# Kernel optimization log

Measured on AMD Instinct MI355X. Metric: run time of the kernel, lower is better.

The kernel has to match this reference:

```python
import jax, jax.numpy as jnp
import numpy as np

B, CIN, K, H, W = 8, 256, 128, 112, 112


def setup_inputs() -> dict:
    key = jax.random.key(0)
    k1, k2, k3, k4 = jax.random.split(key, 4)
    return {
        "x": jax.random.normal(k1, (B, CIN, H, W), jnp.float32),
        "linComb": jax.random.uniform(k2, (K, CIN), dtype=jnp.float32),
        "geoParams": jax.random.uniform(k3, (K, 2, 3), dtype=jnp.float32),
        "boxParams": jax.random.uniform(k4, (K, 2, 3), dtype=jnp.float32),
    }


def _affine_sample(img, theta):
    """F.affine_grid + F.grid_sample (bilinear, zeros padding, align_corners=False).
    img: [B, K, H, W] (one feature channel per geometric channel k)
    theta: [K, 2, 3] affine params, shared across batch.
    """
    Bn, Kn, Hn, Wn = img.shape
    # normalized output coords (align_corners=False pixel centers)
    xs = (2.0 * jnp.arange(Wn, dtype=img.dtype) + 1.0) / Wn - 1.0
    ys = (2.0 * jnp.arange(Hn, dtype=img.dtype) + 1.0) / Hn - 1.0
    gxv, gyv = jnp.meshgrid(xs, ys)  # [H, W]
    coords = jnp.stack([gxv, gyv, jnp.ones_like(gxv)], axis=-1)  # [H, W, 3]
    grid = jnp.einsum('kij,hwj->khwi', theta, coords)  # [K, H, W, 2] (x, y)
    # unnormalize to input pixel space
    ix = ((grid[..., 0] + 1.0) * Wn - 1.0) * 0.5
    iy = ((grid[..., 1] + 1.0) * Hn - 1.0) * 0.5
    x0 = jnp.floor(ix)
    y0 = jnp.floor(iy)
    wx1 = ix - x0
    wx0 = 1.0 - wx1
    wy1 = iy - y0
    wy0 = 1.0 - wy1
    imgf = img.reshape(Bn, Kn, Hn * Wn)

    def gather(xc, yc, w):
        valid = (xc >= 0) & (xc <= Wn - 1) & (yc >= 0) & (yc <= Hn - 1)
        xi = jnp.clip(xc, 0, Wn - 1).astype(jnp.int32)
        yi = jnp.clip(yc, 0, Hn - 1).astype(jnp.int32)
        idx = (yi * Wn + xi).reshape(Kn, Hn * Wn)
        vals = jnp.take_along_axis(
            imgf, jnp.broadcast_to(idx[None], (Bn, Kn, Hn * Wn)), axis=2
        ).reshape(Bn, Kn, Hn, Wn)
        return vals * (w * valid.astype(img.dtype))[None]

    out = (gather(x0, y0, wx0 * wy0)
           + gather(x0 + 1.0, y0, wx1 * wy0)
           + gather(x0, y0 + 1.0, wx0 * wy1)
           + gather(x0 + 1.0, y0 + 1.0, wx1 * wy1))
    return out


def reference(x, linComb, geoParams, boxParams):
    # channel-weighted sum: (x.unsqueeze(1) * linComb).sum(dim=2) == 1x1-conv GEMM
    comb = jnp.einsum('bchw,kc->bkhw', x, linComb)  # [B, K, H, W]
    box = _affine_sample(jnp.ones_like(comb), boxParams)
    warped = _affine_sample(comb, geoParams)
    finalPred = warped * box
    return (finalPred, warped, box)
```

## Files before the change

kernel.cpp:

```cpp
#include <hip/hip_runtime.h>
#include <hip/hip_bf16.h>

namespace {
constexpr int Bn = 8, Cn = 256, Kn = 128, Hn = 112, Wn = 112;
constexpr int Pn = Hn * Wn;
constexpr long long NOUT = (long long)Bn * Kn * Pn;

typedef __attribute__((ext_vector_type(8))) short bf16x8;
typedef __attribute__((ext_vector_type(4))) float f32x4;

__device__ inline unsigned short f2bf(float f) {
  __hip_bfloat16 h = __float2bfloat16(f);
  return __builtin_bit_cast(unsigned short, h);
}
__device__ inline unsigned int pack2bf(float a, float b) {
  return (unsigned int)f2bf(a) | ((unsigned int)f2bf(b) << 16);
}
__device__ inline float bf2f(unsigned short u) {
  return __bfloat162float(__builtin_bit_cast(__hip_bfloat16, u));
}
}

__global__ __launch_bounds__(256) void prep_lcQ(const float* __restrict__ lc,
                                                unsigned int* __restrict__ lcQ) {
  int idx = blockIdx.x * 256 + threadIdx.x;
  int r = idx & 3;
  int l15 = (idx >> 2) & 15;
  int l4 = (idx >> 6) & 3;
  int ks = (idx >> 8) & 7;
  int s = idx >> 11;
  int c2 = s * 16 + l4 * 4 + r;
  int k = ks * 16 + l15;
  lcQ[idx] = pack2bf(lc[k * Cn + 2 * c2], lc[k * Cn + 2 * c2 + 1]);
}

__global__ __launch_bounds__(256) void gemm_mfma(const float* __restrict__ x,
                                                 const uint4* __restrict__ lcQ4,
                                                 unsigned short* __restrict__ combh) {
  const int tid = threadIdx.x;
  const int wid = tid >> 6;
  const int lane = tid & 63;
  const int l15 = lane & 15, l4 = lane >> 4;
  const int b = blockIdx.x / 196;
  const int p0 = (blockIdx.x % 196) * 64 + wid * 16;
  const float* xb = x + (size_t)b * Cn * Pn;

  f32x4 acc[8];
#pragma unroll
  for (int ks = 0; ks < 8; ++ks) acc[ks] = (f32x4)(0.f);

#pragma unroll 2
  for (int s = 0; s < 8; ++s) {
    const float* src = xb + (size_t)(32 * s + l4 * 8) * Pn + (p0 + l15);
    float v[8];
#pragma unroll
    for (int j = 0; j < 8; ++j) v[j] = src[(size_t)j * Pn];
    union { unsigned int u[4]; bf16x8 vv; } au;
#pragma unroll
    for (int r = 0; r < 4; ++r) au.u[r] = pack2bf(v[2 * r], v[2 * r + 1]);
#pragma unroll
    for (int ks = 0; ks < 8; ++ks) {
      union { uint4 q; bf16x8 vv; } bu;
      bu.q = lcQ4[((s * 8 + ks) * 4 + l4) * 16 + l15];
      acc[ks] = __builtin_amdgcn_mfma_f32_16x16x32_bf16(au.vv, bu.vv, acc[ks], 0, 0, 0);
    }
  }

#pragma unroll
  for (int ks = 0; ks < 8; ++ks) {
    const size_t o = ((size_t)b * Kn + ks * 16 + l15) * Pn + p0 + l4 * 4;
    uint2 st;
    st.x = pack2bf(acc[ks][0], acc[ks][1]);
    st.y = pack2bf(acc[ks][2], acc[ks][3]);
    *reinterpret_cast<uint2*>(combh + o) = st;
  }
}

__global__ __launch_bounds__(256) void sample_lds(const unsigned short* __restrict__ comb,
                                                  const float* __restrict__ geo,
                                                  const float* __restrict__ boxp,
                                                  float* __restrict__ outF,
                                                  float* __restrict__ outW,
                                                  float* __restrict__ outB) {
  __shared__ __align__(16) unsigned short img[Pn];
  const int bx = blockIdx.x;
  const int k = bx & 127;
  const int tid = threadIdx.x;

  {
    const uint4* src = reinterpret_cast<const uint4*>(comb + (size_t)bx * Pn);
    uint4* dst = reinterpret_cast<uint4*>(img);
    for (int i = tid; i < Pn / 8; i += 256) dst[i] = src[i];
  }
  __syncthreads();

  const float* g = geo + k * 6;
  const float* t = boxp + k * 6;
  const float g0 = g[0], g1 = g[1], g2 = g[2], g3 = g[3], g4 = g[4], g5 = g[5];
  const float t0 = t[0], t1 = t[1], t2 = t[2], t3 = t[3], t4 = t[4], t5 = t[5];
  const size_t obase = (size_t)bx * Pn;

  for (int pp = tid; pp < Pn; pp += 256) {
    const int h = pp / Wn;
    const int w = pp - h * Wn;
    const float xn = (2.f * w + 1.f) / (float)Wn - 1.f;
    const float yn = (2.f * h + 1.f) / (float)Hn - 1.f;

    float ix = ((g0 * xn + g1 * yn + g2 + 1.f) * Wn - 1.f) * 0.5f;
    float iy = ((g3 * xn + g4 * yn + g5 + 1.f) * Hn - 1.f) * 0.5f;
    float x0f = floorf(ix), y0f = floorf(iy);
    float wx1 = ix - x0f, wx0 = 1.f - wx1;
    float wy1 = iy - y0f, wy0 = 1.f - wy1;
    float vx0 = (x0f >= 0.f && x0f <= (float)(Wn - 1)) ? 1.f : 0.f;
    float vx1 = (x0f + 1.f >= 0.f && x0f + 1.f <= (float)(Wn - 1)) ? 1.f : 0.f;
    float vy0 = (y0f >= 0.f && y0f <= (float)(Hn - 1)) ? 1.f : 0.f;
    float vy1 = (y0f + 1.f >= 0.f && y0f + 1.f <= (float)(Hn - 1)) ? 1.f : 0.f;
    int x0i = (int)fminf(fmaxf(x0f, 0.f), (float)(Wn - 1));
    int x1i = (int)fminf(fmaxf(x0f + 1.f, 0.f), (float)(Wn - 1));
    int y0i = (int)fminf(fmaxf(y0f, 0.f), (float)(Hn - 1));
    int y1i = (int)fminf(fmaxf(y0f + 1.f, 0.f), (float)(Hn - 1));
    float w00 = wx0 * wy0 * vx0 * vy0;
    float w01 = wx1 * wy0 * vx1 * vy0;
    float w10 = wx0 * wy1 * vx0 * vy1;
    float w11 = wx1 * wy1 * vx1 * vy1;
    int i00 = y0i * Wn + x0i, i01 = y0i * Wn + x1i;
    int i10 = y1i * Wn + x0i, i11 = y1i * Wn + x1i;

    float bix = ((t0 * xn + t1 * yn + t2 + 1.f) * Wn - 1.f) * 0.5f;
    float biy = ((t3 * xn + t4 * yn + t5 + 1.f) * Hn - 1.f) * 0.5f;
    float bx0 = floorf(bix), by0 = floorf(biy);
    float bwx1 = bix - bx0, bwx0 = 1.f - bwx1;
    float bwy1 = biy - by0, bwy0 = 1.f - bwy1;
    float bvx0 = (bx0 >= 0.f && bx0 <= (float)(Wn - 1)) ? 1.f : 0.f;
    float bvx1 = (bx0 + 1.f >= 0.f && bx0 + 1.f <= (float)(Wn - 1)) ? 1.f : 0.f;
    float bvy0 = (by0 >= 0.f && by0 <= (float)(Hn - 1)) ? 1.f : 0.f;
    float bvy1 = (by0 + 1.f >= 0.f && by0 + 1.f <= (float)(Hn - 1)) ? 1.f : 0.f;
    float bv = bwx0 * bwy0 * bvx0 * bvy0 + bwx1 * bwy0 * bvx1 * bvy0 +
               bwx0 * bwy1 * bvx0 * bvy1 + bwx1 * bwy1 * bvx1 * bvy1;

    float v = w00 * bf2f(img[i00]) + w01 * bf2f(img[i01]) +
              w10 * bf2f(img[i10]) + w11 * bf2f(img[i11]);
    const size_t o = obase + pp;
    __builtin_nontemporal_store(v, &outW[o]);
    __builtin_nontemporal_store(bv, &outB[o]);
    __builtin_nontemporal_store(v * bv, &outF[o]);
  }
}

extern "C" void kernel_launch(void* const* d_in, const int* in_sizes, int n_in,
                              void* d_out, int out_size, void* d_ws, size_t ws_size,
                              hipStream_t stream) {
  (void)in_sizes; (void)n_in; (void)out_size;
  const float* x = (const float*)d_in[0];
  const float* lc = (const float*)d_in[1];
  const float* geo = (const float*)d_in[2];
  const float* boxp = (const float*)d_in[3];
  float* outF = (float*)d_out;
  float* outW = outF + NOUT;
  float* outB = outW + NOUT;

  unsigned int* lcQ = (unsigned int*)outB;

  const size_t comb_bytes = (size_t)NOUT * sizeof(unsigned short);
  const bool use_ws = ws_size >= comb_bytes;
  unsigned short* combh = use_ws ? (unsigned short*)d_ws : (unsigned short*)outF;

  prep_lcQ<<<64, 256, 0, stream>>>(lc, lcQ);
  gemm_mfma<<<Bn * (Pn / 64), 256, 0, stream>>>(x, (const uint4*)lcQ, combh);
  sample_lds<<<Bn * Kn, 256, 0, stream>>>(combh, geo, boxp, outF, outW, outB);
}
```

Before: 278.6 us.

## Stage GEMM input tiles through double-buffered LDS with vectorized float4 loads

The GEMM kernel now loads each 32-channel by 64-pixel slab of x cooperatively with float4 global loads into a double-buffered shared-memory tile. Each wave then reads its A fragment from LDS instead of doing scalar strided global loads. The next slab is prefetched into registers while the current slab's MFMAs run. This widens global memory transactions and overlaps load latency with compute, at the cost of a block-wide barrier per step and added LDS traffic.

```diff
diff --git a/kernel.cpp b/kernel.cpp
--- a/kernel.cpp
+++ b/kernel.cpp
@@ -37,24 +37,43 @@
 __global__ __launch_bounds__(256) void gemm_mfma(const float* __restrict__ x,
                                                  const uint4* __restrict__ lcQ4,
                                                  unsigned short* __restrict__ combh) {
+  __shared__ __align__(16) float xs[2][32][64];
   const int tid = threadIdx.x;
   const int wid = tid >> 6;
   const int lane = tid & 63;
   const int l15 = lane & 15, l4 = lane >> 4;
   const int b = blockIdx.x / 196;
-  const int p0 = (blockIdx.x % 196) * 64 + wid * 16;
-  const float* xb = x + (size_t)b * Cn * Pn;
+  const int p0 = (blockIdx.x % 196) * 64;
+  const float* xb = x + (size_t)b * Cn * Pn + p0;
+
+  const int srow0 = tid >> 4;
+  const int scol = (tid & 15) * 4;
+  const int srow1 = srow0 + 16;
 
   f32x4 acc[8];
 #pragma unroll
   for (int ks = 0; ks < 8; ++ks) acc[ks] = (f32x4)(0.f);
 
-#pragma unroll 2
+  {
+    float4 v0 = *reinterpret_cast<const float4*>(xb + (size_t)srow0 * Pn + scol);
+    float4 v1 = *reinterpret_cast<const float4*>(xb + (size_t)srow1 * Pn + scol);
+    *reinterpret_cast<float4*>(&xs[0][srow0][scol]) = v0;
+    *reinterpret_cast<float4*>(&xs[0][srow1][scol]) = v1;
+  }
+  __syncthreads();
+
   for (int s = 0; s < 8; ++s) {
-    const float* src = xb + (size_t)(32 * s + l4 * 8) * Pn + (p0 + l15);
+    const int cur = s & 1;
+    float4 n0, n1;
+    if (s < 7) {
+      const float* g = xb + (size_t)(32 * (s + 1)) * Pn;
+      n0 = *reinterpret_cast<const float4*>(g + (size_t)srow0 * Pn + scol);
+      n1 = *reinterpret_cast<const float4*>(g + (size_t)srow1 * Pn + scol);
+    }
+
     float v[8];
 #pragma unroll
-    for (int j = 0; j < 8; ++j) v[j] = src[(size_t)j * Pn];
+    for (int j = 0; j < 8; ++j) v[j] = xs[cur][l4 * 8 + j][wid * 16 + l15];
     union { unsigned int u[4]; bf16x8 vv; } au;
 #pragma unroll
     for (int r = 0; r < 4; ++r) au.u[r] = pack2bf(v[2 * r], v[2 * r + 1]);
@@ -64,11 +83,17 @@
       bu.q = lcQ4[((s * 8 + ks) * 4 + l4) * 16 + l15];
       acc[ks] = __builtin_amdgcn_mfma_f32_16x16x32_bf16(au.vv, bu.vv, acc[ks], 0, 0, 0);
     }
+
+    if (s < 7) {
+      *reinterpret_cast<float4*>(&xs[cur ^ 1][srow0][scol]) = n0;
+      *reinterpret_cast<float4*>(&xs[cur ^ 1][srow1][scol]) = n1;
+    }
+    __syncthreads();
   }
 
 #pragma unroll
   for (int ks = 0; ks < 8; ++ks) {
-    const size_t o = ((size_t)b * Kn + ks * 16 + l15) * Pn + p0 + l4 * 4;
+    const size_t o = ((size_t)b * Kn + ks * 16 + l15) * Pn + p0 + wid * 16 + l4 * 4;
     uint2 st;
     st.x = pack2bf(acc[ks][0], acc[ks][1]);
     st.y = pack2bf(acc[ks][2], acc[ks][3]);
```

Result: no change. 274.7 us (-1.4%).

## Stage GEMM x tiles through double-buffered LDS and vectorize sampler stores

Applied to the files above, without the earlier changes.

The GEMM kernel now processes 128 pixels per block. Each wave computes two 16-pixel sub-tiles, so every lcQ fragment load is reused across two MFMAs. x is loaded with coalesced float4 reads into a double-buffered LDS tile, and the next channel slab is prefetched while the current one is being consumed. The sampler kernel handles two adjacent pixels per thread and writes its three outputs as 2-wide nontemporal stores. This adds LDS use, more accumulators and a barrier every iteration, in exchange for cutting strided scalar global loads and halving the number of GEMM blocks.

```diff
diff --git a/kernel.cpp b/kernel.cpp
--- a/kernel.cpp
+++ b/kernel.cpp
@@ -8,6 +8,7 @@
 
 typedef __attribute__((ext_vector_type(8))) short bf16x8;
 typedef __attribute__((ext_vector_type(4))) float f32x4;
+typedef __attribute__((ext_vector_type(2))) float f32x2;
 
 __device__ inline unsigned short f2bf(float f) {
   __hip_bfloat16 h = __float2bfloat16(f);
@@ -37,42 +38,83 @@
 __global__ __launch_bounds__(256) void gemm_mfma(const float* __restrict__ x,
                                                  const uint4* __restrict__ lcQ4,
                                                  unsigned short* __restrict__ combh) {
+  __shared__ __align__(16) float xs[2][32][128];
   const int tid = threadIdx.x;
   const int wid = tid >> 6;
   const int lane = tid & 63;
   const int l15 = lane & 15, l4 = lane >> 4;
-  const int b = blockIdx.x / 196;
-  const int p0 = (blockIdx.x % 196) * 64 + wid * 16;
-  const float* xb = x + (size_t)b * Cn * Pn;
-
-  f32x4 acc[8];
-#pragma unroll
-  for (int ks = 0; ks < 8; ++ks) acc[ks] = (f32x4)(0.f);
-
-#pragma unroll 2
+  const int b = blockIdx.x / 98;
+  const int p0 = (blockIdx.x % 98) * 128;
+  const float* xb = x + (size_t)b * Cn * Pn + p0;
+
+  int srow[4], scol[4];
+#pragma unroll
+  for (int q = 0; q < 4; ++q) {
+    int fidx = q * 256 + tid;
+    srow[q] = fidx >> 5;
+    scol[q] = (fidx & 31) * 4;
+  }
+
+  f32x4 acc[8][2];
+#pragma unroll
+  for (int ks = 0; ks < 8; ++ks)
+#pragma unroll
+    for (int ps = 0; ps < 2; ++ps) acc[ks][ps] = (f32x4)(0.f);
+
+#pragma unroll
+  for (int q = 0; q < 4; ++q) {
+    float4 v = *reinterpret_cast<const float4*>(xb + (size_t)srow[q] * Pn + scol[q]);
+    *reinterpret_cast<float4*>(&xs[0][srow[q]][scol[q]]) = v;
+  }
+  __syncthreads();
+
   for (int s = 0; s < 8; ++s) {
-    const float* src = xb + (size_t)(32 * s + l4 * 8) * Pn + (p0 + l15);
-    float v[8];
-#pragma unroll
-    for (int j = 0; j < 8; ++j) v[j] = src[(size_t)j * Pn];
-    union { unsigned int u[4]; bf16x8 vv; } au;
-#pragma unroll
-    for (int r = 0; r < 4; ++r) au.u[r] = pack2bf(v[2 * r], v[2 * r + 1]);
+    const int cur = s & 1;
+    float4 nv[4];
+    if (s < 7) {
+      const float* g = xb + (size_t)(32 * (s + 1)) * Pn;
+#pragma unroll
+      for (int q = 0; q < 4; ++q)
+        nv[q] = *reinterpret_cast<const float4*>(g + (size_t)srow[q] * Pn + scol[q]);
+    }
+
+    union { unsigned int u[4]; bf16x8 vv; } au[2];
+#pragma unroll
+    for (int ps = 0; ps < 2; ++ps) {
+      float v[8];
+#pragma unroll
+      for (int j = 0; j < 8; ++j) v[j] = xs[cur][l4 * 8 + j][wid * 32 + ps * 16 + l15];
+#pragma unroll
+      for (int r = 0; r < 4; ++r) au[ps].u[r] = pack2bf(v[2 * r], v[2 * r + 1]);
+    }
 #pragma unroll
     for (int ks = 0; ks < 8; ++ks) {
       union { uint4 q; bf16x8 vv; } bu;
       bu.q = lcQ4[((s * 8 + ks) * 4 + l4) * 16 + l15];
-      acc[ks] = __builtin_amdgcn_mfma_f32_16x16x32_bf16(au.vv, bu.vv, acc[ks], 0, 0, 0);
-    }
+#pragma unroll
+      for (int ps = 0; ps < 2; ++ps)
+        acc[ks][ps] = __builtin_amdgcn_mfma_f32_16x16x32_bf16(au[ps].vv, bu.vv, acc[ks][ps], 0, 0, 0);
+    }
+
+    if (s < 7) {
+#pragma unroll
+      for (int q = 0; q < 4; ++q)
+        *reinterpret_cast<float4*>(&xs[cur ^ 1][srow[q]][scol[q]]) = nv[q];
+    }
+    __syncthreads();
   }
 
 #pragma unroll
   for (int ks = 0; ks < 8; ++ks) {
-    const size_t o = ((size_t)b * Kn + ks * 16 + l15) * Pn + p0 + l4 * 4;
-    uint2 st;
-    st.x = pack2bf(acc[ks][0], acc[ks][1]);
-    st.y = pack2bf(acc[ks][2], acc[ks][3]);
-    *reinterpret_cast<uint2*>(combh + o) = st;
+    const size_t krow = ((size_t)b * Kn + ks * 16 + l15) * Pn;
+#pragma unroll
+    for (int ps = 0; ps < 2; ++ps) {
+      const int p = p0 + wid * 32 + ps * 16 + l4 * 4;
+      uint2 st;
+      st.x = pack2bf(acc[ks][ps][0], acc[ks][ps][1]);
+      st.y = pack2bf(acc[ks][ps][2], acc[ks][ps][3]);
+      *reinterpret_cast<uint2*>(combh + krow + p) = st;
+    }
   }
 }
 
@@ -100,50 +142,60 @@
   const float t0 = t[0], t1 = t[1], t2 = t[2], t3 = t[3], t4 = t[4], t5 = t[5];
   const size_t obase = (size_t)bx * Pn;
 
-  for (int pp = tid; pp < Pn; pp += 256) {
-    const int h = pp / Wn;
-    const int w = pp - h * Wn;
-    const float xn = (2.f * w + 1.f) / (float)Wn - 1.f;
+  for (int i = 0; i < 25; ++i) {
+    const int idx = tid + i * 256;
+    if (idx >= Pn / 2) break;
+    const int p = 2 * idx;
+    const int h = idx / 56;
+    const int w0 = p - h * Wn;
     const float yn = (2.f * h + 1.f) / (float)Hn - 1.f;
 
-    float ix = ((g0 * xn + g1 * yn + g2 + 1.f) * Wn - 1.f) * 0.5f;
-    float iy = ((g3 * xn + g4 * yn + g5 + 1.f) * Hn - 1.f) * 0.5f;
-    float x0f = floorf(ix), y0f = floorf(iy);
-    float wx1 = ix - x0f, wx0 = 1.f - wx1;
-    float wy1 = iy - y0f, wy0 = 1.f - wy1;
-    float vx0 = (x0f >= 0.f && x0f <= (float)(Wn - 1)) ? 1.f : 0.f;
-    float vx1 = (x0f + 1.f >= 0.f && x0f + 1.f <= (float)(Wn - 1)) ? 1.f : 0.f;
-    float vy0 = (y0f >= 0.f && y0f <= (float)(Hn - 1)) ? 1.f : 0.f;
-    float vy1 = (y0f + 1.f >= 0.f && y0f + 1.f <= (float)(Hn - 1)) ? 1.f : 0.f;
-    int x0i = (int)fminf(fmaxf(x0f, 0.f), (float)(Wn - 1));
-    int x1i = (int)fminf(fmaxf(x0f + 1.f, 0.f), (float)(Wn - 1));
-    int y0i = (int)fminf(fmaxf(y0f, 0.f), (float)(Hn - 1));
-    int y1i = (int)fminf(fmaxf(y0f + 1.f, 0.f), (float)(Hn - 1));
-    float w00 = wx0 * wy0 * vx0 * vy0;
-    float w01 = wx1 * wy0 * vx1 * vy0;
-    float w10 = wx0 * wy1 * vx0 * vy1;
-    float w11 = wx1 * wy1 * vx1 * vy1;
-    int i00 = y0i * Wn + x0i, i01 = y0i * Wn + x1i;
-    int i10 = y1i * Wn + x0i, i11 = y1i * Wn + x1i;
-
-    float bix = ((t0 * xn + t1 * yn + t2 + 1.f) * Wn - 1.f) * 0.5f;
-    float biy = ((t3 * xn + t4 * yn + t5 + 1.f) * Hn - 1.f) * 0.5f;
-    float bx0 = floorf(bix), by0 = floorf(biy);
-    float bwx1 = bix - bx0, bwx0 = 1.f - bwx1;
-    float bwy1 = biy - by0, bwy0 = 1.f - bwy1;
-    float bvx0 = (bx0 >= 0.f && bx0 <= (float)(Wn - 1)) ? 1.f : 0.f;
-    float bvx1 = (bx0 + 1.f >= 0.f && bx0 + 1.f <= (float)(Wn - 1)) ? 1.f : 0.f;
-    float bvy0 = (by0 >= 0.f && by0 <= (float)(Hn - 1)) ? 1.f : 0.f;
-    float bvy1 = (by0 + 1.f >= 0.f && by0 + 1.f <= (float)(Hn - 1)) ? 1.f : 0.f;
-    float bv = bwx0 * bwy0 * bvx0 * bvy0 + bwx1 * bwy0 * bvx1 * bvy0 +
-               bwx0 * bwy1 * bvx0 * bvy1 + bwx1 * bwy1 * bvx1 * bvy1;
-
-    float v = w00 * bf2f(img[i00]) + w01 * bf2f(img[i01]) +
-              w10 * bf2f(img[i10]) + w11 * bf2f(img[i11]);
-    const size_t o = obase + pp;
-    __builtin_nontemporal_store(v, &outW[o]);
-    __builtin_nontemporal_store(bv, &outB[o]);
-    __builtin_nontemporal_store(v * bv, &outF[o]);
+    float vv[2], bb[2];
+#pragma unroll
+    for (int e = 0; e < 2; ++e) {
+      const int w = w0 + e;
+      const float xn = (2.f * w + 1.f) / (float)Wn - 1.f;
+
+      float ix = ((g0 * xn + g1 * yn + g2 + 1.f) * Wn - 1.f) * 0.5f;
+      float iy = ((g3 * xn + g4 * yn + g5 + 1.f) * Hn - 1.f) * 0.5f;
+      float x0f = floorf(ix), y0f = floorf(iy);
+      float wx1 = ix - x0f, wx0 = 1.f - wx1;
+      float wy1 = iy - y0f, wy0 = 1.f - wy1;
+      float vx0 = (x0f >= 0.f && x0f <= (float)(Wn - 1)) ? 1.f : 0.f;
+      float vx1 = (x0f + 1.f >= 0.f && x0f + 1.f <= (float)(Wn - 1)) ? 1.f : 0.f;
+      float vy0 = (y0f >= 0.f && y0f <= (float)(Hn - 1)) ? 1.f : 0.f;
+      float vy1 = (y0f + 1.f >= 0.f && y0f + 1.f <= (float)(Hn - 1)) ? 1.f : 0.f;
+      int x0i = (int)fminf(fmaxf(x0f, 0.f), (float)(Wn - 1));
+      int x1i = (int)fminf(fmaxf(x0f + 1.f, 0.f), (float)(Wn - 1));
+      int y0i = (int)fminf(fmaxf(y0f, 0.f), (float)(Hn - 1));
+      int y1i = (int)fminf(fmaxf(y0f + 1.f, 0.f), (float)(Hn - 1));
+      float w00 = wx0 * wy0 * vx0 * vy0;
+      float w01 = wx1 * wy0 * vx1 * vy0;
+      float w10 = wx0 * wy1 * vx0 * vy1;
+      float w11 = wx1 * wy1 * vx1 * vy1;
+      vv[e] = w00 * bf2f(img[y0i * Wn + x0i]) + w01 * bf2f(img[y0i * Wn + x1i]) +
+              w10 * bf2f(img[y1i * Wn + x0i]) + w11 * bf2f(img[y1i * Wn + x1i]);
+
+      float bix = ((t0 * xn + t1 * yn + t2 + 1.f) * Wn - 1.f) * 0.5f;
+      float biy = ((t3 * xn + t4 * yn + t5 + 1.f) * Hn - 1.f) * 0.5f;
+      float bx0 = floorf(bix), by0 = floorf(biy);
+      float bwx1 = bix - bx0, bwx0 = 1.f - bwx1;
+      float bwy1 = biy - by0, bwy0 = 1.f - bwy1;
+      float bvx0 = (bx0 >= 0.f && bx0 <= (float)(Wn - 1)) ? 1.f : 0.f;
+      float bvx1 = (bx0 + 1.f >= 0.f && bx0 + 1.f <= (float)(Wn - 1)) ? 1.f : 0.f;
+      float bvy0 = (by0 >= 0.f && by0 <= (float)(Hn - 1)) ? 1.f : 0.f;
+      float bvy1 = (by0 + 1.f >= 0.f && by0 + 1.f <= (float)(Hn - 1)) ? 1.f : 0.f;
+      bb[e] = bwx0 * bwy0 * bvx0 * bvy0 + bwx1 * bwy0 * bvx1 * bvy0 +
+              bwx0 * bwy1 * bvx0 * bvy1 + bwx1 * bwy1 * bvx1 * bvy1;
+    }
+
+    const size_t o = obase + p;
+    f32x2 wv; wv.x = vv[0]; wv.y = vv[1];
+    f32x2 bv; bv.x = bb[0]; bv.y = bb[1];
+    f32x2 fv; fv.x = vv[0] * bb[0]; fv.y = vv[1] * bb[1];
+    __builtin_nontemporal_store(wv, reinterpret_cast<f32x2*>(&outW[o]));
+    __builtin_nontemporal_store(bv, reinterpret_cast<f32x2*>(&outB[o]));
+    __builtin_nontemporal_store(fv, reinterpret_cast<f32x2*>(&outF[o]));
   }
 }
 
@@ -166,6 +218,6 @@
   unsigned short* combh = use_ws ? (unsigned short*)d_ws : (unsigned short*)outF;
 
   prep_lcQ<<<64, 256, 0, stream>>>(lc, lcQ);
-  gemm_mfma<<<Bn * (Pn / 64), 256, 0, stream>>>(x, (const uint4*)lcQ, combh);
+  gemm_mfma<<<Bn * (Pn / 128), 256, 0, stream>>>(x, (const uint4*)lcQ, combh);
   sample_lds<<<Bn * Kn, 256, 0, stream>>>(combh, geo, boxp, outF, outW, outB);
 }
```

New measurement: 313.3 us. +12.4%, slower.
